# Kernel tuning notes

Hardware: AMD Instinct MI355X
Metric: run time of the kernel (lower is better)

Reference implementation:

```python
import jax, jax.numpy as jnp
import numpy as np

DIM = 2048
DIM_HEAD = 64
HEADS = 16
FF_MULT = 4
LORA_R = 8
ATTN_INNER = DIM_HEAD * HEADS            # 1024
FF_INNER = DIM * FF_MULT                 # 8192
FUSED_DIMS = (ATTN_INNER, DIM_HEAD, DIM_HEAD, FF_INNER * 2)
B, N = 2, 2048


def setup_inputs() -> dict:
    key = jax.random.key(0)
    ks = jax.random.split(key, 12)
    s = 0.02
    inp = {
        "x": jax.random.normal(ks[0], (B, N, DIM), dtype=jnp.float32),
        "gamma": jnp.ones((DIM,), dtype=jnp.float32),
        "w_fused": jax.random.normal(ks[1], (DIM, sum(FUSED_DIMS)), dtype=jnp.float32) * s,
        "w_attn_out": jax.random.normal(ks[2], (ATTN_INNER, DIM), dtype=jnp.float32) * s,
        "w_ff_out": jax.random.normal(ks[3], (FF_INNER, DIM), dtype=jnp.float32) * s,
        "lora_q_a": jax.random.normal(ks[4], (DIM, LORA_R), dtype=jnp.float32) * s,
        "lora_q_b": jax.random.normal(ks[5], (LORA_R, ATTN_INNER), dtype=jnp.float32) * s,
        "lora_k_a": jax.random.normal(ks[6], (DIM, LORA_R), dtype=jnp.float32) * s,
        "lora_k_b": jax.random.normal(ks[7], (LORA_R, DIM_HEAD), dtype=jnp.float32) * s,
        "lora_v_a": jax.random.normal(ks[8], (DIM, LORA_R), dtype=jnp.float32) * s,
        "lora_v_b": jax.random.normal(ks[9], (LORA_R, DIM_HEAD), dtype=jnp.float32) * s,
        "lora_o_a": jax.random.normal(ks[10], (ATTN_INNER, LORA_R), dtype=jnp.float32) * s,
        "lora_o_b": jax.random.normal(ks[11], (LORA_R, DIM), dtype=jnp.float32) * s,
    }
    return inp


def _rotate_half(x):
    x1, x2 = jnp.split(x, 2, axis=-1)
    return jnp.concatenate((-x2, x1), axis=-1)


def _rope(pos, t):
    return t * jnp.cos(pos) + _rotate_half(t) * jnp.sin(pos)


def _forward(x, gamma, w_fused, w_attn_out, w_ff_out,
             lora_q_a, lora_q_b, lora_k_a, lora_k_b,
             lora_v_a, lora_v_b, lora_o_a, lora_o_b):
    b, n, d = x.shape
    # LayerNorm (beta = 0)
    mu = jnp.mean(x, axis=-1, keepdims=True)
    var = jnp.var(x, axis=-1, keepdims=True)
    xn = (x - mu) * jax.lax.rsqrt(var + 1e-5) * gamma

    fused = xn @ w_fused
    i0, i1, i2 = np.cumsum(FUSED_DIMS)[:3]
    q, k, v, ff = fused[..., :i0], fused[..., i0:i1], fused[..., i1:i2], fused[..., i2:]

    # LoRA additive terms
    q = q + (xn @ lora_q_a) @ lora_q_b
    k = k + (xn @ lora_k_a) @ lora_k_b
    v = v + (xn @ lora_v_a) @ lora_v_b

    q = q.reshape(b, n, HEADS, DIM_HEAD).transpose(0, 2, 1, 3)  # b h n d
    q = q * (DIM_HEAD ** -0.5)

    # rotary embedding: pos (n, dim_head)
    inv_freq = 1.0 / (10000.0 ** (jnp.arange(0, DIM_HEAD, 2, dtype=jnp.float32) / DIM_HEAD))
    freqs = jnp.arange(n, dtype=jnp.float32)[:, None] * inv_freq[None, :]
    pos = jnp.concatenate((freqs, freqs), axis=-1)
    q = _rope(pos, q)
    k = _rope(pos, k)  # k is b n d (multi-query, single kv head)

    sim = jnp.einsum('bhid,bjd->bhij', q, k)
    causal = jnp.triu(jnp.ones((n, n), dtype=bool), k=1)
    sim = jnp.where(causal, -jnp.finfo(sim.dtype).max, sim)
    attn = jax.nn.softmax(sim, axis=-1)
    out = jnp.einsum('bhij,bjd->bhid', attn, v)
    out = out.transpose(0, 2, 1, 3).reshape(b, n, ATTN_INNER)

    attn_out = out @ w_attn_out + (out @ lora_o_a) @ lora_o_b

    # SwiGLU: chunk -> (x_ff, gate); silu(gate) * x_ff
    x_ff, gate = jnp.split(ff, 2, axis=-1)
    ff_out = (jax.nn.silu(gate) * x_ff) @ w_ff_out

    return attn_out + ff_out


def reference(x, gamma, w_fused, w_attn_out, w_ff_out,
              lora_q_a, lora_q_b, lora_k_a, lora_k_b,
              lora_v_a, lora_v_b, lora_o_a, lora_o_b):
    return _forward(x, gamma, w_fused, w_attn_out, w_ff_out,
                    lora_q_a, lora_q_b, lora_k_a, lora_k_b,
                    lora_v_a, lora_v_b, lora_o_a, lora_o_b)
```

## Files before the change

kernel.cpp:

```cpp
#include <hip/hip_runtime.h>
#include <cstdint>


typedef __bf16 bf16_t;
typedef __bf16 bf16x8 __attribute__((ext_vector_type(8)));
typedef float f32x4 __attribute__((ext_vector_type(4)));

#define LOG2E 1.44269504088896340736f
#define LOG2_10K 13.287712379549449f

__device__ __forceinline__ void gload_lds16(const void* g, void* l) {
  __builtin_amdgcn_global_load_lds(
      (__attribute__((address_space(1))) void*)(uintptr_t)g,
      (__attribute__((address_space(3))) void*)(uint32_t)(uintptr_t)l,
      16, 0, 0);
}

__device__ __forceinline__ f32x4 mfma16(bf16x8 a, bf16x8 b, f32x4 c) {
  return __builtin_amdgcn_mfma_f32_16x16x32_bf16(a, b, c, 0, 0, 0);
}

__global__ __launch_bounds__(256) void ln_kernel(
    const float* __restrict__ x, const float* __restrict__ gamma,
    bf16_t* __restrict__ xn)
{
  const int row = blockIdx.x;
  const int t = threadIdx.x;
  const float4* xr = (const float4*)(x + (size_t)row * 2048);
  float4 a = xr[t * 2];
  float4 b = xr[t * 2 + 1];
  float s  = a.x + a.y + a.z + a.w + b.x + b.y + b.z + b.w;
  float ss = a.x*a.x + a.y*a.y + a.z*a.z + a.w*a.w
           + b.x*b.x + b.y*b.y + b.z*b.z + b.w*b.w;
  #pragma unroll
  for (int m = 1; m < 64; m <<= 1) {
    s  += __shfl_xor(s, m);
    ss += __shfl_xor(ss, m);
  }
  __shared__ float red[8];
  const int wave = t >> 6, lane = t & 63;
  if (lane == 0) { red[wave] = s; red[4 + wave] = ss; }
  __syncthreads();
  const float stot  = red[0] + red[1] + red[2] + red[3];
  const float sstot = red[4] + red[5] + red[6] + red[7];
  const float mu  = stot * (1.f / 2048.f);
  const float var = sstot * (1.f / 2048.f) - mu * mu;
  const float rs  = rsqrtf(var + 1e-5f);
  float v[8] = {a.x, a.y, a.z, a.w, b.x, b.y, b.z, b.w};
  bf16x8 o;
  #pragma unroll
  for (int e = 0; e < 8; ++e)
    o[e] = (bf16_t)((v[e] - mu) * rs * gamma[t * 8 + e]);
  *(bf16x8*)(xn + (size_t)row * 2048 + t * 8) = o;
}

__global__ __launch_bounds__(256) void transpose_wf_kernel(
    const float* __restrict__ w,
    const float* __restrict__ qa, const float* __restrict__ qb,
    const float* __restrict__ ka, const float* __restrict__ kb,
    const float* __restrict__ va, const float* __restrict__ vb,
    bf16_t* __restrict__ wfT)
{
  __shared__ float tile[64][65];
  const int t  = threadIdx.x;
  const int n0 = blockIdx.x * 64;
  const int k0 = blockIdx.y * 64;
  #pragma unroll
  for (int it = 0; it < 4; ++it) {
    const int kr = (t >> 4) + it * 16;
    const float4 vv = *(const float4*)(w + (size_t)(k0 + kr) * 17536 + n0 + (t & 15) * 4);
    tile[kr][(t & 15) * 4 + 0] = vv.x;
    tile[kr][(t & 15) * 4 + 1] = vv.y;
    tile[kr][(t & 15) * 4 + 2] = vv.z;
    tile[kr][(t & 15) * 4 + 3] = vv.w;
  }
  __syncthreads();
  const float* la = nullptr; const float* lb = nullptr;
  int nbo = 0, ldlb = 0;
  if (n0 < 1024)      { la = qa; lb = qb; nbo = n0;        ldlb = 1024; }
  else if (n0 < 1088) { la = ka; lb = kb; nbo = n0 - 1024; ldlb = 64;   }
  else if (n0 < 1152) { la = va; lb = vb; nbo = n0 - 1088; ldlb = 64;   }
  #pragma unroll
  for (int it = 0; it < 2; ++it) {
    const int nl = (t >> 3) + it * 32;
    const int kl = (t & 7) * 8;
    float vals[8];
    #pragma unroll
    for (int e = 0; e < 8; ++e) vals[e] = tile[kl + e][nl];
    if (la) {
      float bc[8];
      #pragma unroll
      for (int r = 0; r < 8; ++r) bc[r] = lb[r * ldlb + nbo + nl];
      #pragma unroll
      for (int e = 0; e < 8; ++e) {
        const float* ar = la + (size_t)(k0 + kl + e) * 8;
        float d = 0.f;
        #pragma unroll
        for (int r = 0; r < 8; ++r) d += ar[r] * bc[r];
        vals[e] += d;
      }
    }
    bf16x8 o;
    #pragma unroll
    for (int e = 0; e < 8; ++e) o[e] = (bf16_t)vals[e];
    *(bf16x8*)(wfT + (size_t)(n0 + nl) * 2048 + k0 + kl) = o;
  }
}

__global__ __launch_bounds__(256) void transpose_w2_kernel(
    const float* __restrict__ wff,
    const float* __restrict__ watt,
    const float* __restrict__ oa, const float* __restrict__ ob,
    bf16_t* __restrict__ w2T)
{
  __shared__ float tile[64][65];
  const int t  = threadIdx.x;
  const int n0 = blockIdx.x * 64;
  const int k0 = blockIdx.y * 64;
  const bool isatt = (k0 >= 8192);
  const float* src = isatt ? (watt + (size_t)(k0 - 8192) * 2048)
                           : (wff + (size_t)k0 * 2048);
  #pragma unroll
  for (int it = 0; it < 4; ++it) {
    const int kr = (t >> 4) + it * 16;
    const float4 vv = *(const float4*)(src + (size_t)kr * 2048 + n0 + (t & 15) * 4);
    tile[kr][(t & 15) * 4 + 0] = vv.x;
    tile[kr][(t & 15) * 4 + 1] = vv.y;
    tile[kr][(t & 15) * 4 + 2] = vv.z;
    tile[kr][(t & 15) * 4 + 3] = vv.w;
  }
  __syncthreads();
  #pragma unroll
  for (int it = 0; it < 2; ++it) {
    const int nl = (t >> 3) + it * 32;
    const int kl = (t & 7) * 8;
    float vals[8];
    #pragma unroll
    for (int e = 0; e < 8; ++e) vals[e] = tile[kl + e][nl];
    if (isatt) {
      float bc[8];
      #pragma unroll
      for (int r = 0; r < 8; ++r) bc[r] = ob[r * 2048 + n0 + nl];
      #pragma unroll
      for (int e = 0; e < 8; ++e) {
        const float* ar = oa + (size_t)(k0 - 8192 + kl + e) * 8;
        float d = 0.f;
        #pragma unroll
        for (int r = 0; r < 8; ++r) d += ar[r] * bc[r];
        vals[e] += d;
      }
    }
    bf16x8 o;
    #pragma unroll
    for (int e = 0; e < 8; ++e) o[e] = (bf16_t)vals[e];
    *(bf16x8*)(w2T + (size_t)(n0 + nl) * 9216 + k0 + kl) = o;
  }
}

__device__ __forceinline__ void gemm_core_128x128(
    const bf16_t* __restrict__ A, int ldA, int m0,
    const bf16_t* __restrict__ BT, int ldB, int n0,
    int K, bf16_t* As, bf16_t* Bs, f32x4* acc)
{
  const int t = threadIdx.x;
  const int wave = t >> 6;
  const int lane = t & 63;
  const int quad = lane >> 4;
  const int ln15 = lane & 15;
  const int wm = wave & 1, wn = wave >> 1;

  const bf16_t* gA = A + (size_t)(m0 + (t >> 2)) * ldA + ((t & 3) << 3);
  const bf16_t* gB = BT + (size_t)(n0 + (t >> 2)) * ldB + ((t & 3) << 3);
  char* lA = (char*)As + wave * 1024;
  char* lB = (char*)Bs + wave * 1024;
  const size_t sA64 = (size_t)64 * ldA;
  const size_t sB64 = (size_t)64 * ldB;
  const int aoff = (wm * 64 + ln15) * 32 + quad * 8;
  const int boff = (wn * 64 + ln15) * 32 + quad * 8;

  for (int kt = 0; kt < K; kt += 32) {
    gload_lds16(gA,        lA);
    gload_lds16(gA + sA64, lA + 4096);
    gload_lds16(gB,        lB);
    gload_lds16(gB + sB64, lB + 4096);
    gA += 32;
    gB += 32;
    __syncthreads();
    bf16x8 a0 = *(const bf16x8*)(As + aoff);
    bf16x8 a1 = *(const bf16x8*)(As + aoff + 512);
    bf16x8 a2 = *(const bf16x8*)(As + aoff + 1024);
    bf16x8 a3 = *(const bf16x8*)(As + aoff + 1536);
    bf16x8 b0 = *(const bf16x8*)(Bs + boff);
    bf16x8 b1 = *(const bf16x8*)(Bs + boff + 512);
    bf16x8 b2 = *(const bf16x8*)(Bs + boff + 1024);
    bf16x8 b3 = *(const bf16x8*)(Bs + boff + 1536);
    acc[0]  = mfma16(a0, b0, acc[0]);
    acc[1]  = mfma16(a0, b1, acc[1]);
    acc[2]  = mfma16(a0, b2, acc[2]);
    acc[3]  = mfma16(a0, b3, acc[3]);
    acc[4]  = mfma16(a1, b0, acc[4]);
    acc[5]  = mfma16(a1, b1, acc[5]);
    acc[6]  = mfma16(a1, b2, acc[6]);
    acc[7]  = mfma16(a1, b3, acc[7]);
    acc[8]  = mfma16(a2, b0, acc[8]);
    acc[9]  = mfma16(a2, b1, acc[9]);
    acc[10] = mfma16(a2, b2, acc[10]);
    acc[11] = mfma16(a2, b3, acc[11]);
    acc[12] = mfma16(a3, b0, acc[12]);
    acc[13] = mfma16(a3, b1, acc[13]);
    acc[14] = mfma16(a3, b2, acc[14]);
    acc[15] = mfma16(a3, b3, acc[15]);
    __syncthreads();
  }
}

__device__ __forceinline__ void gemm_core_dual(
    const bf16_t* gA, const bf16_t* gB0, const bf16_t* gB1,
    int ldA, int ldB, int K,
    bf16_t* As, bf16_t* B0s, bf16_t* B1s,
    f32x4* acc0, f32x4* acc1)
{
  const int t = threadIdx.x;
  const int wave = t >> 6;
  const int lane = t & 63;
  const int quad = lane >> 4;
  const int ln15 = lane & 15;
  const int wm = wave & 1, wn = wave >> 1;

  char* lA = (char*)As + wave * 1024;
  char* l0 = (char*)B0s + wave * 1024;
  char* l1 = (char*)B1s + wave * 1024;
  const size_t sA64 = (size_t)64 * ldA;
  const size_t sB64 = (size_t)64 * ldB;
  const int aoff = (wm * 64 + ln15) * 32 + quad * 8;
  const int boff = (wn * 64 + ln15) * 32 + quad * 8;

  for (int kt = 0; kt < K; kt += 32) {
    gload_lds16(gA,         lA);
    gload_lds16(gA + sA64,  lA + 4096);
    gload_lds16(gB0,        l0);
    gload_lds16(gB0 + sB64, l0 + 4096);
    gload_lds16(gB1,        l1);
    gload_lds16(gB1 + sB64, l1 + 4096);
    gA += 32; gB0 += 32; gB1 += 32;
    __syncthreads();
    bf16x8 a0 = *(const bf16x8*)(As + aoff);
    bf16x8 a1 = *(const bf16x8*)(As + aoff + 512);
    bf16x8 a2 = *(const bf16x8*)(As + aoff + 1024);
    bf16x8 a3 = *(const bf16x8*)(As + aoff + 1536);
    bf16x8 p0 = *(const bf16x8*)(B0s + boff);
    bf16x8 p1 = *(const bf16x8*)(B0s + boff + 512);
    bf16x8 p2 = *(const bf16x8*)(B0s + boff + 1024);
    bf16x8 p3 = *(const bf16x8*)(B0s + boff + 1536);
    bf16x8 q0 = *(const bf16x8*)(B1s + boff);
    bf16x8 q1 = *(const bf16x8*)(B1s + boff + 512);
    bf16x8 q2 = *(const bf16x8*)(B1s + boff + 1024);
    bf16x8 q3 = *(const bf16x8*)(B1s + boff + 1536);
    acc0[0]  = mfma16(a0, p0, acc0[0]);
    acc0[1]  = mfma16(a0, p1, acc0[1]);
    acc0[2]  = mfma16(a0, p2, acc0[2]);
    acc0[3]  = mfma16(a0, p3, acc0[3]);
    acc1[0]  = mfma16(a0, q0, acc1[0]);
    acc1[1]  = mfma16(a0, q1, acc1[1]);
    acc1[2]  = mfma16(a0, q2, acc1[2]);
    acc1[3]  = mfma16(a0, q3, acc1[3]);
    acc0[4]  = mfma16(a1, p0, acc0[4]);
    acc0[5]  = mfma16(a1, p1, acc0[5]);
    acc0[6]  = mfma16(a1, p2, acc0[6]);
    acc0[7]  = mfma16(a1, p3, acc0[7]);
    acc1[4]  = mfma16(a1, q0, acc1[4]);
    acc1[5]  = mfma16(a1, q1, acc1[5]);
    acc1[6]  = mfma16(a1, q2, acc1[6]);
    acc1[7]  = mfma16(a1, q3, acc1[7]);
    acc0[8]  = mfma16(a2, p0, acc0[8]);
    acc0[9]  = mfma16(a2, p1, acc0[9]);
    acc0[10] = mfma16(a2, p2, acc0[10]);
    acc0[11] = mfma16(a2, p3, acc0[11]);
    acc1[8]  = mfma16(a2, q0, acc1[8]);
    acc1[9]  = mfma16(a2, q1, acc1[9]);
    acc1[10] = mfma16(a2, q2, acc1[10]);
    acc1[11] = mfma16(a2, q3, acc1[11]);
    acc0[12] = mfma16(a3, p0, acc0[12]);
    acc0[13] = mfma16(a3, p1, acc0[13]);
    acc0[14] = mfma16(a3, p2, acc0[14]);
    acc0[15] = mfma16(a3, p3, acc0[15]);
    acc1[12] = mfma16(a3, q0, acc1[12]);
    acc1[13] = mfma16(a3, q1, acc1[13]);
    acc1[14] = mfma16(a3, q2, acc1[14]);
    acc1[15] = mfma16(a3, q3, acc1[15]);
    __syncthreads();
  }
}

__global__ __launch_bounds__(256, 2) void gemm1_qkv_kernel(
    const bf16_t* __restrict__ xn, const bf16_t* __restrict__ wfT,
    bf16_t* __restrict__ Q, bf16_t* __restrict__ K, bf16_t* __restrict__ Vt)
{
  __shared__ __align__(16) bf16_t As[128 * 32];
  __shared__ __align__(16) bf16_t B0s[128 * 32];
  __shared__ __align__(16) bf16_t B1s[128 * 32];
  const int m0 = blockIdx.x * 128;
  const int y = blockIdx.y;
  const int t = threadIdx.x;
  const int wave = t >> 6, lane = t & 63;
  const int quad = lane >> 4, ln15 = lane & 15;
  const int wm = wave & 1, wn = wave >> 1;

  const int rb = m0 + wm * 64 + quad * 4;
  const float invf0 = exp2f(-(float)ln15 * (LOG2_10K / 32.0f));
  const float invf1 = exp2f(-(float)(16 + ln15) * (LOG2_10K / 32.0f));

  if (y < 4) {
    const bf16_t* gA  = xn  + (size_t)(m0 + (t >> 2)) * 2048 + ((t & 3) << 3);
    const bf16_t* gB0 = wfT + (size_t)(y * 256 + (t >> 2)) * 2048 + ((t & 3) << 3);
    const bf16_t* gB1 = wfT + (size_t)(y * 256 + 128 + (t >> 2)) * 2048 + ((t & 3) << 3);
    f32x4 acc0[16], acc1[16];
    #pragma unroll
    for (int f = 0; f < 16; ++f) {
      acc0[f] = (f32x4){0.f, 0.f, 0.f, 0.f};
      acc1[f] = (f32x4){0.f, 0.f, 0.f, 0.f};
    }
    gemm_core_dual(gA, gB0, gB1, 2048, 2048, 2048, As, B0s, B1s, acc0, acc1);
    #pragma unroll
    for (int half = 0; half < 2; ++half) {
      const f32x4* acc = half ? acc1 : acc0;
      const int hd = y * 4 + half * 2 + wn;
      #pragma unroll
      for (int i = 0; i < 4; ++i) {
        #pragma unroll
        for (int rr = 0; rr < 4; ++rr) {
          const int row = rb + i * 16 + rr;
          const int b = row >> 11, n = row & 2047;
          const float fn = (float)n;
          float s0, c0, s1, c1;
          __sincosf(fn * invf0, &s0, &c0);
          __sincosf(fn * invf1, &s1, &c1);
          float vals[4];
          #pragma unroll
          for (int j = 0; j < 4; ++j) vals[j] = acc[i * 4 + j][rr];
          #pragma unroll
          for (int j = 0; j < 4; ++j) {
            const float rot = (j < 2) ? -vals[j + 2] : vals[j - 2];
            const float c = (j & 1) ? c1 : c0;
            const float s = (j & 1) ? s1 : s0;
            const float o = (vals[j] * c + rot * s) * 0.125f;
            Q[(((size_t)b * 16 + hd) * 2048 + n) * 64 + j * 16 + ln15] = (bf16_t)o;
          }
        }
      }
    }
  } else {
    f32x4 acc[16];
    #pragma unroll
    for (int f = 0; f < 16; ++f) acc[f] = (f32x4){0.f, 0.f, 0.f, 0.f};
    gemm_core_128x128(xn, 2048, m0, wfT, 2048, 1024, 2048, As, B0s, acc);
    const bool is_k = (wn == 0);
    #pragma unroll
    for (int i = 0; i < 4; ++i) {
      #pragma unroll
      for (int rr = 0; rr < 4; ++rr) {
        const int row = rb + i * 16 + rr;
        const int b = row >> 11, n = row & 2047;
        float vals[4];
        #pragma unroll
        for (int j = 0; j < 4; ++j) vals[j] = acc[i * 4 + j][rr];
        if (is_k) {
          const float fn = (float)n;
          float s0, c0, s1, c1;
          __sincosf(fn * invf0, &s0, &c0);
          __sincosf(fn * invf1, &s1, &c1);
          #pragma unroll
          for (int j = 0; j < 4; ++j) {
            const float rot = (j < 2) ? -vals[j + 2] : vals[j - 2];
            const float c = (j & 1) ? c1 : c0;
            const float s = (j & 1) ? s1 : s0;
            K[((size_t)b * 2048 + n) * 64 + j * 16 + ln15] = (bf16_t)(vals[j] * c + rot * s);
          }
        } else {
          #pragma unroll
          for (int j = 0; j < 4; ++j)
            Vt[((size_t)b * 64 + j * 16 + ln15) * 2048 + n] = (bf16_t)vals[j];
        }
      }
    }
  }
}

__global__ __launch_bounds__(512, 2) void gemm1_ff_kernel(
    const bf16_t* __restrict__ xn, const bf16_t* __restrict__ wfT,
    bf16_t* __restrict__ A2)
{
  __shared__ __align__(16) char lds[131072];
  const int m0 = blockIdx.x * 256;
  const int c0 = blockIdx.y * 128;
  const int t = threadIdx.x;
  const int w = t >> 6, lane = t & 63;
  const int quad = lane >> 4, ln15 = lane & 15;
  const int wm = w & 1, wn = w >> 1;

  const int p  = w * 64 + lane;
  const int r  = p >> 2;
  const int cl = (p & 3) ^ ((r >> 1) & 3);
  const bf16_t* gA = xn + (size_t)(m0 + r) * 2048 + cl * 8;
  const int r2 = r + 128;
  const int cm0 = c0 + ((r  >> 5) << 4) + (r  & 15);
  const int cm1 = c0 + ((r2 >> 5) << 4) + (r2 & 15);
  const int wr0 = ((r  >> 4) & 1) ? (1152 + cm0) : (9344 + cm0);
  const int wr1 = ((r2 >> 4) & 1) ? (1152 + cm1) : (9344 + cm1);
  const bf16_t* gB0 = wfT + (size_t)wr0 * 2048 + cl * 8;
  const bf16_t* gB1 = wfT + (size_t)wr1 * 2048 + cl * 8;

  const int ro = ln15 * 64 + ((quad ^ ((ln15 >> 1) & 3)) * 16);

  f32x4 acc[8][4];
  #pragma unroll
  for (int mf = 0; mf < 8; ++mf)
    #pragma unroll
    for (int nf = 0; nf < 4; ++nf)
      acc[mf][nf] = (f32x4){0.f, 0.f, 0.f, 0.f};

  #pragma unroll
  for (int pt = 0; pt < 3; ++pt) {
    char* lA = lds + pt * 16384 + w * 1024;
    gload_lds16(gA,                        lA);
    gload_lds16(gA + (size_t)128 * 2048,   lA + 8192);
    char* lB = lds + 65536 + pt * 16384 + w * 1024;
    gload_lds16(gB0, lB);
    gload_lds16(gB1, lB + 8192);
    gA += 32; gB0 += 32; gB1 += 32;
  }
  asm volatile("s_waitcnt vmcnt(8)" ::: "memory");
  __builtin_amdgcn_s_barrier();

  for (int tt = 0; tt < 64; ++tt) {
    const int s  = tt & 3;
    const int s3 = (tt + 3) & 3;
    const bool st = (tt < 61);
    bf16x8 a[4], b[4];
    #pragma unroll
    for (int mf = 0; mf < 4; ++mf)
      a[mf] = *(const bf16x8*)(lds + s * 16384 + wm * 8192 + mf * 1024 + ro);
    #pragma unroll
    for (int nf = 0; nf < 4; ++nf)
      b[nf] = *(const bf16x8*)(lds + 65536 + s * 16384 + wn * 4096 + nf * 1024 + ro);
    if (st) {
      char* lA = lds + s3 * 16384 + w * 1024;
      gload_lds16(gA,                      lA);
      gload_lds16(gA + (size_t)128 * 2048, lA + 8192);
    }
    __builtin_amdgcn_s_barrier();
    __builtin_amdgcn_s_setprio(1);
    #pragma unroll
    for (int mf = 0; mf < 4; ++mf)
      #pragma unroll
      for (int nf = 0; nf < 4; ++nf)
        acc[mf][nf] = mfma16(a[mf], b[nf], acc[mf][nf]);
    __builtin_amdgcn_s_setprio(0);
    bf16x8 a2[4];
    #pragma unroll
    for (int mf = 0; mf < 4; ++mf)
      a2[mf] = *(const bf16x8*)(lds + s * 16384 + wm * 8192 + (4 + mf) * 1024 + ro);
    if (st) {
      char* lB = lds + 65536 + s3 * 16384 + w * 1024;
      gload_lds16(gB0, lB);
      gload_lds16(gB1, lB + 8192);
      gA += 32; gB0 += 32; gB1 += 32;
    }
    __builtin_amdgcn_s_barrier();
    __builtin_amdgcn_s_setprio(1);
    #pragma unroll
    for (int mf = 0; mf < 4; ++mf)
      #pragma unroll
      for (int nf = 0; nf < 4; ++nf)
        acc[4 + mf][nf] = mfma16(a2[mf], b[nf], acc[4 + mf][nf]);
    __builtin_amdgcn_s_setprio(0);
    asm volatile("s_waitcnt vmcnt(8)" ::: "memory");
    __builtin_amdgcn_s_barrier();
  }

  const int row0 = m0 + wm * 128 + quad * 4;
  const int col0 = c0 + wn * 32 + ln15;
  #pragma unroll
  for (int mf = 0; mf < 8; ++mf)
    #pragma unroll
    for (int rr = 0; rr < 4; ++rr) {
      bf16_t* dst = A2 + (size_t)(row0 + mf * 16 + rr) * 9216 + col0;
      #pragma unroll
      for (int j = 0; j < 2; ++j) {
        const float g  = acc[mf][2 * j][rr];
        const float xv = acc[mf][2 * j + 1][rr];
        dst[j * 16] = (bf16_t)(xv * (g / (1.f + exp2f(-g * LOG2E))));
      }
    }
}

__global__ __launch_bounds__(512, 2) void gemm2_kernel(
    const bf16_t* __restrict__ A2, const bf16_t* __restrict__ w2T,
    float* __restrict__ out)
{
  __shared__ __align__(16) char lds[98304];
  const int m0 = blockIdx.x * 256;
  const int n0 = blockIdx.y * 128;
  const int t = threadIdx.x;
  const int w = t >> 6, lane = t & 63;
  const int quad = lane >> 4, ln15 = lane & 15;
  const int wm = w & 3, wn = w >> 2;

  const int p  = w * 64 + lane;
  const int r  = p >> 2;
  const int cl = (p & 3) ^ ((r >> 1) & 3);
  const bf16_t* gA = A2  + (size_t)(m0 + r) * 9216 + cl * 8;
  const bf16_t* gB = w2T + (size_t)(n0 + r) * 9216 + cl * 8;

  const int ro = ln15 * 64 + ((quad ^ ((ln15 >> 1) & 3)) * 16);

  f32x4 acc[4][4];
  #pragma unroll
  for (int mf = 0; mf < 4; ++mf)
    #pragma unroll
    for (int nf = 0; nf < 4; ++nf)
      acc[mf][nf] = (f32x4){0.f, 0.f, 0.f, 0.f};

  #pragma unroll
  for (int pt = 0; pt < 3; ++pt) {
    char* lA = lds + pt * 16384 + w * 1024;
    gload_lds16(gA,                      lA);
    gload_lds16(gA + (size_t)128 * 9216, lA + 8192);
    gload_lds16(gB, lds + 65536 + pt * 8192 + w * 1024);
    gA += 32; gB += 32;
  }
  asm volatile("s_waitcnt vmcnt(6)" ::: "memory");
  __builtin_amdgcn_s_barrier();

  for (int tt = 0; tt < 288; ++tt) {
    const int s = tt & 3;
    bf16x8 a[4], b[4];
    #pragma unroll
    for (int mf = 0; mf < 4; ++mf)
      a[mf] = *(const bf16x8*)(lds + s * 16384 + wm * 4096 + mf * 1024 + ro);
    #pragma unroll
    for (int nf = 0; nf < 4; ++nf)
      b[nf] = *(const bf16x8*)(lds + 65536 + s * 8192 + wn * 4096 + nf * 1024 + ro);
    if (tt < 285) {
      const int s3 = (tt + 3) & 3;
      char* lA = lds + s3 * 16384 + w * 1024;
      gload_lds16(gA,                      lA);
      gload_lds16(gA + (size_t)128 * 9216, lA + 8192);
      gload_lds16(gB, lds + 65536 + s3 * 8192 + w * 1024);
      gA += 32; gB += 32;
    }
    __builtin_amdgcn_s_barrier();
    __builtin_amdgcn_s_setprio(1);
    #pragma unroll
    for (int mf = 0; mf < 4; ++mf)
      #pragma unroll
      for (int nf = 0; nf < 4; ++nf)
        acc[mf][nf] = mfma16(a[mf], b[nf], acc[mf][nf]);
    __builtin_amdgcn_s_setprio(0);
    asm volatile("s_waitcnt vmcnt(6)" ::: "memory");
    __builtin_amdgcn_s_barrier();
  }

  const int row0 = m0 + wm * 64 + quad * 4;
  const int col0 = n0 + wn * 64 + ln15;
  #pragma unroll
  for (int mf = 0; mf < 4; ++mf)
    #pragma unroll
    for (int rr = 0; rr < 4; ++rr) {
      float* dst = out + (size_t)(row0 + mf * 16 + rr) * 2048 + col0;
      #pragma unroll
      for (int nf = 0; nf < 4; ++nf)
        dst[nf * 16] = acc[mf][nf][rr];
    }
}

__global__ __launch_bounds__(256, 2) void attn_kernel(
    const bf16_t* __restrict__ Q, const bf16_t* __restrict__ Kg_,
    const bf16_t* __restrict__ Vt, bf16_t* __restrict__ A2)
{
  __shared__ __align__(16) bf16_t Qs[64 * 64];
  __shared__ __align__(16) bf16_t Ks[64 * 64];
  __shared__ __align__(16) bf16_t Vs[64 * 64];
  __shared__ __align__(16) bf16_t Ps[64 * 64];
  const int pidx = blockIdx.x, bh = blockIdx.y;
  const int b = bh >> 4, h = bh & 15;
  const int t = threadIdx.x;
  const int wave = t >> 6, lane = t & 63;
  const int quad = lane >> 4, ln15 = lane & 15;

  const bf16_t* Kg = Kg_ + (size_t)b * 2048 * 64;
  const bf16_t* Vg = Vt + (size_t)b * 64 * 2048;

  for (int hlf = 0; hlf < 2; ++hlf) {
    const int qt = hlf ? (31 - pidx) : pidx;
    const int qm0 = qt * 64;
    const bf16_t* Qg = Q + ((size_t)bh * 2048 + qm0) * 64;

    {
      const bf16_t* g = Qg + (size_t)(t >> 3) * 64 + ((t & 7) << 3);
      char* l = (char*)Qs + wave * 1024;
      gload_lds16(g,           l);
      gload_lds16(g + 32 * 64, l + 4096);
    }

    float mstate[4], lstate[4];
    f32x4 o_acc[4];
    #pragma unroll
    for (int rr = 0; rr < 4; ++rr) { mstate[rr] = -1e30f; lstate[rr] = 0.f; }
    #pragma unroll
    for (int jd = 0; jd < 4; ++jd) o_acc[jd] = (f32x4){0.f, 0.f, 0.f, 0.f};

    const int njt = qt + 1;
    for (int jt = 0; jt < njt; ++jt) {
      {
        const bf16_t* kg = Kg + (size_t)(jt * 64 + (t >> 3)) * 64 + ((t & 7) << 3);
        char* lk = (char*)Ks + wave * 1024;
        gload_lds16(kg,           lk);
        gload_lds16(kg + 32 * 64, lk + 4096);
        const bf16_t* vg = Vg + (size_t)(t >> 3) * 2048 + jt * 64 + ((t & 7) << 3);
        char* lv = (char*)Vs + wave * 1024;
        gload_lds16(vg,                   lv);
        gload_lds16(vg + (size_t)32*2048, lv + 4096);
      }
      __syncthreads();

      f32x4 sA[4];
      #pragma unroll
      for (int j = 0; j < 4; ++j) sA[j] = (f32x4){0.f, 0.f, 0.f, 0.f};
      #pragma unroll
      for (int ks = 0; ks < 2; ++ks) {
        bf16x8 aq = *(const bf16x8*)(Qs + (wave * 16 + ln15) * 64 + ks * 32 + quad * 8);
        #pragma unroll
        for (int j = 0; j < 4; ++j) {
          bf16x8 bk = *(const bf16x8*)(Ks + (j * 16 + ln15) * 64 + ks * 32 + quad * 8);
          sA[j] = mfma16(aq, bk, sA[j]);
        }
      }

      const bool needmask = (jt * 64 + 63 > qm0 + wave * 16);
      const int row0 = qm0 + wave * 16 + quad * 4;
      float alpha[4];
      #pragma unroll
      for (int rr = 0; rr < 4; ++rr) {
        const int rowg = row0 + rr;
        if (needmask) {
          #pragma unroll
          for (int j = 0; j < 4; ++j) {
            const int colg = jt * 64 + j * 16 + ln15;
            if (colg > rowg) sA[j][rr] = -1e30f;
          }
        }
        float mx = fmaxf(fmaxf(sA[0][rr], sA[1][rr]),
                         fmaxf(sA[2][rr], sA[3][rr]));
        mx = fmaxf(mx, __shfl_xor(mx, 1));
        mx = fmaxf(mx, __shfl_xor(mx, 2));
        mx = fmaxf(mx, __shfl_xor(mx, 4));
        mx = fmaxf(mx, __shfl_xor(mx, 8));
        const float mold = mstate[rr];
        const float mnew = fmaxf(mold, mx);
        const float al = exp2f((mold - mnew) * LOG2E);
        float rsum = 0.f;
        #pragma unroll
        for (int j = 0; j < 4; ++j) {
          const float p = exp2f((sA[j][rr] - mnew) * LOG2E);
          sA[j][rr] = p;
          rsum += p;
        }
        rsum += __shfl_xor(rsum, 1);
        rsum += __shfl_xor(rsum, 2);
        rsum += __shfl_xor(rsum, 4);
        rsum += __shfl_xor(rsum, 8);
        lstate[rr] = lstate[rr] * al + rsum;
        mstate[rr] = mnew;
        alpha[rr] = al;
      }
      #pragma unroll
      for (int jd = 0; jd < 4; ++jd)
        #pragma unroll
        for (int rr = 0; rr < 4; ++rr)
          o_acc[jd][rr] *= alpha[rr];
      #pragma unroll
      for (int j = 0; j < 4; ++j)
        #pragma unroll
        for (int rr = 0; rr < 4; ++rr)
          Ps[wave * 1024 + (quad * 4 + rr) * 64 + j * 16 + ln15] = (bf16_t)sA[j][rr];

      #pragma unroll
      for (int ks = 0; ks < 2; ++ks) {
        bf16x8 ap = *(const bf16x8*)(Ps + wave * 1024 + ln15 * 64 + ks * 32 + quad * 8);
        #pragma unroll
        for (int jd = 0; jd < 4; ++jd) {
          bf16x8 bv = *(const bf16x8*)(Vs + (jd * 16 + ln15) * 64 + ks * 32 + quad * 8);
          o_acc[jd] = mfma16(ap, bv, o_acc[jd]);
        }
      }
      __syncthreads();
    }

    const int row0 = qm0 + wave * 16 + quad * 4;
    #pragma unroll
    for (int rr = 0; rr < 4; ++rr) {
      const float inv = 1.f / lstate[rr];
      bf16_t* dst = A2 + ((size_t)b * 2048 + row0 + rr) * 9216 + 8192 + h * 64 + ln15;
      #pragma unroll
      for (int jd = 0; jd < 4; ++jd)
        dst[jd * 16] = (bf16_t)(o_acc[jd][rr] * inv);
    }
  }
}

extern "C" void kernel_launch(void* const* d_in, const int* in_sizes, int n_in,
                              void* d_out, int out_size, void* d_ws, size_t ws_size,
                              hipStream_t stream)
{
  const float* x      = (const float*)d_in[0];
  const float* gamma  = (const float*)d_in[1];
  const float* wfused = (const float*)d_in[2];
  const float* watt   = (const float*)d_in[3];
  const float* wff    = (const float*)d_in[4];
  const float* qa     = (const float*)d_in[5];
  const float* qb     = (const float*)d_in[6];
  const float* ka     = (const float*)d_in[7];
  const float* kb     = (const float*)d_in[8];
  const float* va     = (const float*)d_in[9];
  const float* vb     = (const float*)d_in[10];
  const float* oa     = (const float*)d_in[11];
  const float* ob     = (const float*)d_in[12];
  float* out = (float*)d_out;

  char* ws = (char*)d_ws;
  bf16_t* xn  = (bf16_t*)(ws);
  bf16_t* wfT = (bf16_t*)(ws + 16777216);
  bf16_t* w2T = (bf16_t*)(ws + 88604672);
  bf16_t* A2  = (bf16_t*)(ws + 126353408);
  bf16_t* Qr  = (bf16_t*)(ws + 201850880);
  bf16_t* Kr  = (bf16_t*)(ws + 210239488);
  bf16_t* Vtr = (bf16_t*)(ws + 210763776);

  ln_kernel<<<dim3(4096), dim3(256), 0, stream>>>(x, gamma, xn);
  transpose_wf_kernel<<<dim3(274, 32), dim3(256), 0, stream>>>(
      wfused, qa, qb, ka, kb, va, vb, wfT);
  transpose_w2_kernel<<<dim3(32, 144), dim3(256), 0, stream>>>(
      wff, watt, oa, ob, w2T);
  gemm1_qkv_kernel<<<dim3(32, 5), dim3(256), 0, stream>>>(xn, wfT, Qr, Kr, Vtr);
  gemm1_ff_kernel<<<dim3(16, 64), dim3(512), 0, stream>>>(xn, wfT, A2);
  attn_kernel<<<dim3(16, 32), dim3(256), 0, stream>>>(Qr, Kr, Vtr, A2);
  gemm2_kernel<<<dim3(16, 16), dim3(512), 0, stream>>>(A2, w2T, out);
}
```

Baseline: 876.8 us.

## Register double-buffer LDS fragments in FF and output GEMMs with one barrier per step

Restructures the main loops of both big GEMM kernels into a software pipeline. Next-step LDS fragments are read into a second register set while MFMAs run on the current set, and the two barriers per k-step become one (waitcnt plus barrier). This aims to hide LDS read latency and cut synchronisation overhead. In exchange it uses more VGPRs (doubled fragment registers, with 8 A fragments in gemm1), which may cause spills at launch bounds of 512 threads and 2 blocks, and it depends on a tight ring-buffer reuse ordering.

```diff
diff --git a/kernel.cpp b/kernel.cpp
--- a/kernel.cpp
+++ b/kernel.cpp
@@ -386,6 +386,39 @@
   }
 }
 
+
+#define FF_STG() {                                                           \
+    char* lA_ = lds + sst + w * 1024;                                        \
+    gload_lds16(gA, lA_);                                                    \
+    gload_lds16(gA + (size_t)128 * 2048, lA_ + 8192);                        \
+    char* lB_ = lds + 65536 + sst + w * 1024;                                \
+    gload_lds16(gB0, lB_);                                                   \
+    gload_lds16(gB1, lB_ + 8192);                                            \
+    gA += 32; gB0 += 32; gB1 += 32;                                          \
+    sst = (sst + 16384) & 65535; }
+
+#define FF_RD(DA, DB) {                                                      \
+    _Pragma("unroll")                                                        \
+    for (int mf_ = 0; mf_ < 8; ++mf_)                                        \
+      DA[mf_] = *(const bf16x8*)(lds + srd + wm * 8192 + mf_ * 1024 + ro);   \
+    _Pragma("unroll")                                                        \
+    for (int nf_ = 0; nf_ < 4; ++nf_)                                        \
+      DB[nf_] = *(const bf16x8*)(lds + 65536 + srd + wn * 4096 + nf_ * 1024 + ro); \
+    srd = (srd + 16384) & 65535; }
+
+#define FF_MM(SA, SB) {                                                      \
+    __builtin_amdgcn_s_setprio(1);                                           \
+    _Pragma("unroll")                                                        \
+    for (int mf_ = 0; mf_ < 8; ++mf_) {                                      \
+      _Pragma("unroll")                                                      \
+      for (int nf_ = 0; nf_ < 4; ++nf_)                                      \
+        acc[mf_][nf_] = mfma16(SA[mf_], SB[nf_], acc[mf_][nf_]);             \
+    }                                                                        \
+    __builtin_amdgcn_s_setprio(0); }
+
+#define FF_SYNC4() { asm volatile("s_waitcnt vmcnt(4)" ::: "memory");        \
+    __builtin_amdgcn_s_barrier(); }
+
 __global__ __launch_bounds__(512, 2) void gemm1_ff_kernel(
     const bf16_t* __restrict__ xn, const bf16_t* __restrict__ wfT,
     bf16_t* __restrict__ A2)
@@ -419,64 +452,24 @@
     for (int nf = 0; nf < 4; ++nf)
       acc[mf][nf] = (f32x4){0.f, 0.f, 0.f, 0.f};
 
-  #pragma unroll
-  for (int pt = 0; pt < 3; ++pt) {
-    char* lA = lds + pt * 16384 + w * 1024;
-    gload_lds16(gA,                        lA);
-    gload_lds16(gA + (size_t)128 * 2048,   lA + 8192);
-    char* lB = lds + 65536 + pt * 16384 + w * 1024;
-    gload_lds16(gB0, lB);
-    gload_lds16(gB1, lB + 8192);
-    gA += 32; gB0 += 32; gB1 += 32;
-  }
-  asm volatile("s_waitcnt vmcnt(8)" ::: "memory");
+  int sst = 0, srd = 0;
+  #pragma unroll
+  for (int pt = 0; pt < 3; ++pt) FF_STG();
+  FF_SYNC4();
+
+  bf16x8 fA[8], fB[4], nA[8], nB[4];
+  FF_RD(fA, fB);
+
+  for (int i = 0; i < 30; ++i) {
+    FF_STG(); FF_RD(nA, nB); FF_MM(fA, fB); FF_SYNC4();
+    FF_STG(); FF_RD(fA, fB); FF_MM(nA, nB); FF_SYNC4();
+  }
+  FF_STG(); FF_RD(nA, nB); FF_MM(fA, fB); FF_SYNC4();
+  FF_RD(fA, fB); FF_MM(nA, nB);
+  asm volatile("s_waitcnt vmcnt(0)" ::: "memory");
   __builtin_amdgcn_s_barrier();
-
-  for (int tt = 0; tt < 64; ++tt) {
-    const int s  = tt & 3;
-    const int s3 = (tt + 3) & 3;
-    const bool st = (tt < 61);
-    bf16x8 a[4], b[4];
-    #pragma unroll
-    for (int mf = 0; mf < 4; ++mf)
-      a[mf] = *(const bf16x8*)(lds + s * 16384 + wm * 8192 + mf * 1024 + ro);
-    #pragma unroll
-    for (int nf = 0; nf < 4; ++nf)
-      b[nf] = *(const bf16x8*)(lds + 65536 + s * 16384 + wn * 4096 + nf * 1024 + ro);
-    if (st) {
-      char* lA = lds + s3 * 16384 + w * 1024;
-      gload_lds16(gA,                      lA);
-      gload_lds16(gA + (size_t)128 * 2048, lA + 8192);
-    }
-    __builtin_amdgcn_s_barrier();
-    __builtin_amdgcn_s_setprio(1);
-    #pragma unroll
-    for (int mf = 0; mf < 4; ++mf)
-      #pragma unroll
-      for (int nf = 0; nf < 4; ++nf)
-        acc[mf][nf] = mfma16(a[mf], b[nf], acc[mf][nf]);
-    __builtin_amdgcn_s_setprio(0);
-    bf16x8 a2[4];
-    #pragma unroll
-    for (int mf = 0; mf < 4; ++mf)
-      a2[mf] = *(const bf16x8*)(lds + s * 16384 + wm * 8192 + (4 + mf) * 1024 + ro);
-    if (st) {
-      char* lB = lds + 65536 + s3 * 16384 + w * 1024;
-      gload_lds16(gB0, lB);
-      gload_lds16(gB1, lB + 8192);
-      gA += 32; gB0 += 32; gB1 += 32;
-    }
-    __builtin_amdgcn_s_barrier();
-    __builtin_amdgcn_s_setprio(1);
-    #pragma unroll
-    for (int mf = 0; mf < 4; ++mf)
-      #pragma unroll
-      for (int nf = 0; nf < 4; ++nf)
-        acc[4 + mf][nf] = mfma16(a2[mf], b[nf], acc[4 + mf][nf]);
-    __builtin_amdgcn_s_setprio(0);
-    asm volatile("s_waitcnt vmcnt(8)" ::: "memory");
-    __builtin_amdgcn_s_barrier();
-  }
+  FF_RD(nA, nB); FF_MM(fA, fB);
+  FF_MM(nA, nB);
 
   const int row0 = m0 + wm * 128 + quad * 4;
   const int col0 = c0 + wn * 32 + ln15;
@@ -493,6 +486,38 @@
       }
     }
 }
+
+#define G2_STG() {                                                           \
+    char* lA_ = lds + sstA + w * 1024;                                       \
+    gload_lds16(gA, lA_);                                                    \
+    gload_lds16(gA + (size_t)128 * 9216, lA_ + 8192);                        \
+    gload_lds16(gB, lds + 65536 + sstB + w * 1024);                          \
+    gA += 32; gB += 32;                                                      \
+    sstA = (sstA + 16384) & 65535;                                           \
+    sstB = (sstB + 8192) & 32767; }
+
+#define G2_RD(DA, DB) {                                                      \
+    _Pragma("unroll")                                                        \
+    for (int mf_ = 0; mf_ < 4; ++mf_)                                        \
+      DA[mf_] = *(const bf16x8*)(lds + srdA + wm * 4096 + mf_ * 1024 + ro);  \
+    _Pragma("unroll")                                                        \
+    for (int nf_ = 0; nf_ < 4; ++nf_)                                        \
+      DB[nf_] = *(const bf16x8*)(lds + 65536 + srdB + wn * 4096 + nf_ * 1024 + ro); \
+    srdA = (srdA + 16384) & 65535;                                           \
+    srdB = (srdB + 8192) & 32767; }
+
+#define G2_MM(SA, SB) {                                                      \
+    __builtin_amdgcn_s_setprio(1);                                           \
+    _Pragma("unroll")                                                        \
+    for (int mf_ = 0; mf_ < 4; ++mf_) {                                      \
+      _Pragma("unroll")                                                      \
+      for (int nf_ = 0; nf_ < 4; ++nf_)                                      \
+        acc[mf_][nf_] = mfma16(SA[mf_], SB[nf_], acc[mf_][nf_]);             \
+    }                                                                        \
+    __builtin_amdgcn_s_setprio(0); }
+
+#define G2_SYNC3() { asm volatile("s_waitcnt vmcnt(3)" ::: "memory");        \
+    __builtin_amdgcn_s_barrier(); }
 
 __global__ __launch_bounds__(512, 2) void gemm2_kernel(
     const bf16_t* __restrict__ A2, const bf16_t* __restrict__ w2T,
@@ -521,45 +546,24 @@
     for (int nf = 0; nf < 4; ++nf)
       acc[mf][nf] = (f32x4){0.f, 0.f, 0.f, 0.f};
 
-  #pragma unroll
-  for (int pt = 0; pt < 3; ++pt) {
-    char* lA = lds + pt * 16384 + w * 1024;
-    gload_lds16(gA,                      lA);
-    gload_lds16(gA + (size_t)128 * 9216, lA + 8192);
-    gload_lds16(gB, lds + 65536 + pt * 8192 + w * 1024);
-    gA += 32; gB += 32;
-  }
-  asm volatile("s_waitcnt vmcnt(6)" ::: "memory");
+  int sstA = 0, sstB = 0, srdA = 0, srdB = 0;
+  #pragma unroll
+  for (int pt = 0; pt < 3; ++pt) G2_STG();
+  G2_SYNC3();
+
+  bf16x8 fA[4], fB[4], nA[4], nB[4];
+  G2_RD(fA, fB);
+
+  for (int i = 0; i < 142; ++i) {
+    G2_STG(); G2_RD(nA, nB); G2_MM(fA, fB); G2_SYNC3();
+    G2_STG(); G2_RD(fA, fB); G2_MM(nA, nB); G2_SYNC3();
+  }
+  G2_STG(); G2_RD(nA, nB); G2_MM(fA, fB); G2_SYNC3();
+  G2_RD(fA, fB); G2_MM(nA, nB);
+  asm volatile("s_waitcnt vmcnt(0)" ::: "memory");
   __builtin_amdgcn_s_barrier();
-
-  for (int tt = 0; tt < 288; ++tt) {
-    const int s = tt & 3;
-    bf16x8 a[4], b[4];
-    #pragma unroll
-    for (int mf = 0; mf < 4; ++mf)
-      a[mf] = *(const bf16x8*)(lds + s * 16384 + wm * 4096 + mf * 1024 + ro);
-    #pragma unroll
-    for (int nf = 0; nf < 4; ++nf)
-      b[nf] = *(const bf16x8*)(lds + 65536 + s * 8192 + wn * 4096 + nf * 1024 + ro);
-    if (tt < 285) {
-      const int s3 = (tt + 3) & 3;
-      char* lA = lds + s3 * 16384 + w * 1024;
-      gload_lds16(gA,                      lA);
-      gload_lds16(gA + (size_t)128 * 9216, lA + 8192);
-      gload_lds16(gB, lds + 65536 + s3 * 8192 + w * 1024);
-      gA += 32; gB += 32;
-    }
-    __builtin_amdgcn_s_barrier();
-    __builtin_amdgcn_s_setprio(1);
-    #pragma unroll
-    for (int mf = 0; mf < 4; ++mf)
-      #pragma unroll
-      for (int nf = 0; nf < 4; ++nf)
-        acc[mf][nf] = mfma16(a[mf], b[nf], acc[mf][nf]);
-    __builtin_amdgcn_s_setprio(0);
-    asm volatile("s_waitcnt vmcnt(6)" ::: "memory");
-    __builtin_amdgcn_s_barrier();
-  }
+  G2_RD(nA, nB); G2_MM(fA, fB);
+  G2_MM(nA, nB);
 
   const int row0 = m0 + wm * 64 + quad * 4;
   const int col0 = n0 + wn * 64 + ln15;
```

Result: no change. 876.9 us (+0.0%).
